# Kernel tuning notes

Hardware: AMD Instinct MI355X
Metric: run time of the kernel (lower is better)

The kernel has to match this reference:

```python
import jax, jax.numpy as jnp
import numpy as np

B, DEPTH, E, NH, HD = 32, 12, 768, 12, 64
IMG, PS, GRID = 224, 16, 14
N = GRID * GRID + 1  # 197 tokens incl. cls
EPS = 1e-5


def _rel_index(wh, ww):
    # BEiT relative position index, incl. cls-token rows/cols
    coords = np.stack(np.meshgrid(np.arange(wh), np.arange(ww), indexing='ij'))
    cf = coords.reshape(2, -1)
    rc = (cf[:, :, None] - cf[:, None, :]).transpose(1, 2, 0).astype(np.int64)
    rc[:, :, 0] += wh - 1
    rc[:, :, 1] += ww - 1
    rc[:, :, 0] *= 2 * ww - 1
    nrd = (2 * wh - 1) * (2 * ww - 1) + 3
    idx = np.zeros((wh * ww + 1, wh * ww + 1), dtype=np.int32)
    idx[1:, 1:] = rc.sum(-1)
    idx[0, :] = nrd - 3
    idx[:, 0] = nrd - 2
    idx[0, 0] = nrd - 1
    return jnp.asarray(idx)

REL_IDX = _rel_index(GRID, GRID)  # [197,197] int32 constant


def _ln(x, w, b):
    m = x.mean(-1, keepdims=True)
    v = ((x - m) ** 2).mean(-1, keepdims=True)
    return (x - m) * jax.lax.rsqrt(v + EPS) * w + b


def setup_inputs() -> dict:
    key = jax.random.key(0)
    ks = jax.random.split(key, 8)
    s = 0.02
    rn = lambda k, shape: jax.random.normal(k, shape, jnp.float32) * s
    D = DEPTH
    return {
        'x': jax.random.normal(ks[0], (B, 3, IMG, IMG), jnp.float32),
        'patch_w': rn(ks[1], (E, 3 * PS * PS)),
        'patch_b': jnp.zeros((E,), jnp.float32),
        'cls_token': jnp.zeros((1, 1, E), jnp.float32),
        'ln1_w': jnp.ones((D, E), jnp.float32),
        'ln1_b': jnp.zeros((D, E), jnp.float32),
        'qkv_w': rn(ks[2], (D, 3 * E, E)),
        'q_bias': jnp.zeros((D, E), jnp.float32),
        'v_bias': jnp.zeros((D, E), jnp.float32),
        'rel_table': rn(ks[3], (D, (2 * GRID - 1) ** 2 + 3, NH)),
        'proj_w': rn(ks[4], (D, E, E)),
        'proj_b': jnp.zeros((D, E), jnp.float32),
        'ln2_w': jnp.ones((D, E), jnp.float32),
        'ln2_b': jnp.zeros((D, E), jnp.float32),
        'fc1_w': rn(ks[5], (D, 4 * E, E)),
        'fc1_b': jnp.zeros((D, 4 * E), jnp.float32),
        'fc2_w': rn(ks[6], (D, E, 4 * E)),
        'fc2_b': jnp.zeros((D, E), jnp.float32),
        'fcn_w': jnp.ones((E,), jnp.float32),
        'fcn_b': jnp.zeros((E,), jnp.float32),
        'head_w': rn(ks[7], (1000, E)),
        'head_b': jnp.zeros((1000,), jnp.float32),
    }


def reference(x, patch_w, patch_b, cls_token, ln1_w, ln1_b, qkv_w, q_bias,
              v_bias, rel_table, proj_w, proj_b, ln2_w, ln2_b, fc1_w, fc1_b,
              fc2_w, fc2_b, fcn_w, fcn_b, head_w, head_b):
    b = x.shape[0]
    scale = HD ** -0.5
    # patch embed: stride-16 conv == patchify + matmul (weight flattened as [E, C*kh*kw])
    patches = x.reshape(b, 3, GRID, PS, GRID, PS).transpose(0, 2, 4, 1, 3, 5)
    patches = patches.reshape(b, GRID * GRID, 3 * PS * PS)
    tok = patches @ patch_w.T + patch_b
    tok = jnp.concatenate([jnp.broadcast_to(cls_token, (b, 1, E)), tok], axis=1)  # [B,197,E]

    params = dict(ln1_w=ln1_w, ln1_b=ln1_b, qkv_w=qkv_w, q_bias=q_bias,
                  v_bias=v_bias, rel_table=rel_table, proj_w=proj_w,
                  proj_b=proj_b, ln2_w=ln2_w, ln2_b=ln2_b, fc1_w=fc1_w,
                  fc1_b=fc1_b, fc2_w=fc2_w, fc2_b=fc2_b)

    def block(h, p):
        y = _ln(h, p['ln1_w'], p['ln1_b'])
        qkvb = jnp.concatenate([p['q_bias'], jnp.zeros_like(p['q_bias']), p['v_bias']])
        qkv = (y @ p['qkv_w'].T + qkvb).reshape(b, N, 3, NH, HD).transpose(2, 0, 3, 1, 4)
        q, k, v = qkv[0] * scale, qkv[1], qkv[2]  # [B,H,N,hd]
        bias = p['rel_table'][REL_IDX].transpose(2, 0, 1)  # [H,N,N]
        att = jax.nn.softmax(jnp.einsum('bhnd,bhmd->bhnm', q, k) + bias[None], axis=-1)
        o = jnp.einsum('bhnm,bhmd->bhnd', att, v).transpose(0, 2, 1, 3).reshape(b, N, E)
        h = h + o @ p['proj_w'].T + p['proj_b']
        y = _ln(h, p['ln2_w'], p['ln2_b'])
        y = jax.nn.gelu(y @ p['fc1_w'].T + p['fc1_b'], approximate=False)
        return h + y @ p['fc2_w'].T + p['fc2_b'], None

    tok, _ = jax.lax.scan(block, tok, params)
    feat = _ln(tok[:, 1:].mean(axis=1), fcn_w, fcn_b)  # mean pooling over patch tokens
    return feat @ head_w.T + head_b  # [B, 1000]
```

## Files before the change

kernel.cpp:

```cpp
#include <hip/hip_runtime.h>
#include <hip/hip_bf16.h>
#include <math.h>


typedef __hip_bfloat16 bf16;
using short8 = __attribute__((ext_vector_type(8))) short;
using f32x4  = __attribute__((ext_vector_type(4))) float;

#define NTOK 197
#define NHEAD 12
#define NPAD 224

#define S_QKV  1769472
#define S_PROJ 589824
#define S_FC   2359296
#define O_PROJ 1769472
#define O_FC1  2359296
#define O_FC2  4718592
#define W_TOT  7077888

#define GLD(gp, lp) __builtin_amdgcn_global_load_lds( \
    (const unsigned int __attribute__((address_space(1)))*)(gp), \
    (unsigned int __attribute__((address_space(3)))*)(lp), 16, 0, 0)

__global__ __launch_bounds__(256) void cvt_k(const float* __restrict__ src,
                                             bf16* __restrict__ dst, int n8) {
  int t = blockIdx.x * 256 + threadIdx.x;
  if (t >= n8) return;
  size_t i = (size_t)t * 8;
  float4 a = *(const float4*)(src + i);
  float4 b = *(const float4*)(src + i + 4);
  union { short8 v; bf16 e[8]; } u;
  u.e[0] = __float2bfloat16(a.x); u.e[1] = __float2bfloat16(a.y);
  u.e[2] = __float2bfloat16(a.z); u.e[3] = __float2bfloat16(a.w);
  u.e[4] = __float2bfloat16(b.x); u.e[5] = __float2bfloat16(b.y);
  u.e[6] = __float2bfloat16(b.z); u.e[7] = __float2bfloat16(b.w);
  *(short8*)(dst + i) = u.v;
}

__global__ __launch_bounds__(256) void cvt_layer_k(
    const float* __restrict__ qkvw, const float* __restrict__ projw,
    const float* __restrict__ fc1w, const float* __restrict__ fc2w,
    bf16* __restrict__ wl, int d) {
  size_t i = ((size_t)blockIdx.x * 256 + threadIdx.x) * 8;
  if (i >= W_TOT) return;
  const float* src;
  if (i < O_PROJ)      src = qkvw + (size_t)d * S_QKV + i;
  else if (i < O_FC1)  src = projw + (size_t)d * S_PROJ + (i - O_PROJ);
  else if (i < O_FC2)  src = fc1w + (size_t)d * S_FC + (i - O_FC1);
  else                 src = fc2w + (size_t)d * S_FC + (i - O_FC2);
  float4 a = *(const float4*)src;
  float4 b = *(const float4*)(src + 4);
  union { short8 v; bf16 e[8]; } u;
  u.e[0] = __float2bfloat16(a.x); u.e[1] = __float2bfloat16(a.y);
  u.e[2] = __float2bfloat16(a.z); u.e[3] = __float2bfloat16(a.w);
  u.e[4] = __float2bfloat16(b.x); u.e[5] = __float2bfloat16(b.y);
  u.e[6] = __float2bfloat16(b.z); u.e[7] = __float2bfloat16(b.w);
  *(short8*)(wl + i) = u.v;
}

__global__ __launch_bounds__(256) void patchify_k(const float* __restrict__ x,
                                                  bf16* __restrict__ patches) {
  int o = blockIdx.x * 256 + threadIdx.x;
  if (o >= 6272 * 768) return;
  int row = o / 768, col = o % 768;
  int b = row / 196, g = row % 196;
  int gh = g / 14, gw = g % 14;
  int c = col / 256, r = col % 256;
  int ph = r / 16, pw = r % 16;
  patches[o] = __float2bfloat16(
      x[(((size_t)b * 3 + c) * 224 + gh * 16 + ph) * 224 + gw * 16 + pw]);
}

__global__ __launch_bounds__(256) void clsfill_k(const float* __restrict__ cls,
                                                 float* __restrict__ h) {
  int i = blockIdx.x * 256 + threadIdx.x;
  if (i >= 32 * 768) return;
  int b = i / 768, e = i % 768;
  h[((size_t)b * 197) * 768 + e] = cls[e];
}

__global__ __launch_bounds__(256) void vtz_k(bf16* __restrict__ vt) {
  int i = blockIdx.x * 256 + threadIdx.x;
  if (i >= 32 * 12 * 64 * NPAD / 8) return;
  *(short8*)(vt + (size_t)i * 8) = (short8){0,0,0,0,0,0,0,0};
}

__device__ __forceinline__ int ridx(int n, int m) {
  if (n == 0) return (m == 0) ? 731 : 729;
  if (m == 0) return 730;
  int nh = (n - 1) / 14, nw = (n - 1) % 14;
  int mh = (m - 1) / 14, mw = (m - 1) % 14;
  return (nh - mh + 13) * 27 + (nw - mw + 13);
}

__global__ __launch_bounds__(256) void bias_k(const float* __restrict__ rel,
                                              float* __restrict__ biasT,
                                              int layer) {
  int idx = blockIdx.x * 256 + threadIdx.x;
  if (idx >= 12 * NPAD * 256) return;
  int h = idx / (NPAD * 256);
  int rem = idx % (NPAD * 256);
  int m = rem / 256, n = rem % 256;
  float v;
  if (m >= NTOK) {
    v = -1e30f;
  } else {
    int nn = min(n, NTOK - 1);
    v = rel[((size_t)layer * 732 + ridx(nn, m)) * 12 + h];
  }
  biasT[idx] = v;
}

template <int BIASMODE, bool DOGELU, bool DORES, bool REMAP, bool OUTBF16>
__global__ __launch_bounds__(256) void mm_k(
    const bf16* __restrict__ A, const bf16* __restrict__ W,
    const float* __restrict__ bias, const float* __restrict__ bias2,
    const float* __restrict__ Res, void* __restrict__ Cout,
    bf16* __restrict__ vtg, int M, int Nn, int K) {
  __shared__ bf16 As[4096];
  __shared__ bf16 Bs[4096];
  const int tid = threadIdx.x;
  const int lane = tid & 63;
  const int wave = tid >> 6;
  const int wr = wave >> 1, wc = wave & 1;
  const int row0 = blockIdx.x * 128, n0 = blockIdx.y * 128;
  const int srow = tid >> 2;
  const int scol = (tid & 3) * 8;
  const bf16* Ap = A + (size_t)(row0 + srow) * K + scol;
  const bf16* Wp = W + (size_t)(n0 + srow) * K + scol;
  const size_t gstep = (size_t)64 * K;
  const int r16 = lane & 15;
  const int kg = (lane >> 4) * 8;

  f32x4 acc[4][4];
#pragma unroll
  for (int m = 0; m < 4; m++)
#pragma unroll
    for (int n = 0; n < 4; n++) acc[m][n] = (f32x4){0.f, 0.f, 0.f, 0.f};

  for (int k0 = 0; k0 < K; k0 += 32) {
    __syncthreads();
    GLD(Ap, As + tid * 8);
    GLD(Ap + gstep, As + 2048 + tid * 8);
    GLD(Wp, Bs + tid * 8);
    GLD(Wp + gstep, Bs + 2048 + tid * 8);
    Ap += 32; Wp += 32;
    __syncthreads();

    short8 a[4], b[4];
#pragma unroll
    for (int m = 0; m < 4; m++)
      a[m] = *(const short8*)&As[(wr * 64 + m * 16 + r16) * 32 + kg];
#pragma unroll
    for (int n = 0; n < 4; n++)
      b[n] = *(const short8*)&Bs[(wc * 64 + n * 16 + r16) * 32 + kg];
#pragma unroll
    for (int m = 0; m < 4; m++)
#pragma unroll
      for (int n = 0; n < 4; n++)
        acc[m][n] = __builtin_amdgcn_mfma_f32_16x16x32_bf16(a[m], b[n], acc[m][n], 0, 0, 0);
  }

#pragma unroll
  for (int m = 0; m < 4; m++) {
    const int rbase = row0 + wr * 64 + m * 16 + (lane >> 4) * 4;
#pragma unroll
    for (int n = 0; n < 4; n++) {
      const int gc = n0 + wc * 64 + n * 16 + r16;
      f32x4 v = acc[m][n];
#pragma unroll
      for (int j = 0; j < 4; j++) {
        int gr = rbase + j;
        if (gr >= M) continue;
        float val = v[j];
        if (BIASMODE == 0) {
          val += bias[gc];
        } else {
          if (gc < 768) val += bias[gc];
          else if (gc >= 1536) val += bias2[gc - 1536];
        }
        if (DOGELU) val = 0.5f * val * (1.f + erff(val * 0.70710678118654752f));
        if (DORES) val += Res[(size_t)gr * Nn + gc];
        if (BIASMODE == 1 && gc >= 1536) {
          int ob = gr / 197;
          int nn = gr - ob * 197;
          int hd = gc - 1536;
          vtg[(((size_t)ob * 12 + (hd >> 6)) * 64 + (hd & 63)) * NPAD + nn] =
              __float2bfloat16(val);
        } else {
          int orow = REMAP ? (gr + gr / 196 + 1) : gr;
          if (OUTBF16)
            ((bf16*)Cout)[(size_t)orow * Nn + gc] = __float2bfloat16(val);
          else
            ((float*)Cout)[(size_t)orow * Nn + gc] = val;
        }
      }
    }
  }
}

__global__ __launch_bounds__(256) void ln_k(const float* __restrict__ in,
                                            bf16* __restrict__ outp,
                                            const float* __restrict__ w,
                                            const float* __restrict__ b,
                                            int rows) {
  int row = blockIdx.x * 4 + threadIdx.y;
  if (row >= rows) return;
  int lane = threadIdx.x;
  const float* xr = in + (size_t)row * 768;
  float v[12];
  float s = 0.f;
#pragma unroll
  for (int i = 0; i < 12; i++) { v[i] = xr[lane + i * 64]; s += v[i]; }
#pragma unroll
  for (int o = 32; o; o >>= 1) s += __shfl_xor(s, o);
  float mean = s * (1.f / 768.f);
  float var = 0.f;
#pragma unroll
  for (int i = 0; i < 12; i++) { float d = v[i] - mean; var += d * d; }
#pragma unroll
  for (int o = 32; o; o >>= 1) var += __shfl_xor(var, o);
  float rs = rsqrtf(var * (1.f / 768.f) + 1e-5f);
  bf16* orow = outp + (size_t)row * 768;
#pragma unroll
  for (int i = 0; i < 12; i++) {
    int e = lane + i * 64;
    orow[e] = __float2bfloat16((v[i] - mean) * rs * w[e] + b[e]);
  }
}

__device__ __forceinline__ unsigned pkbf(float a, float b) {
  union { bf16 h; unsigned short u; } ua, ub;
  ua.h = __float2bfloat16(a); ub.h = __float2bfloat16(b);
  return ((unsigned)ub.u << 16) | (unsigned)ua.u;
}

__global__ __launch_bounds__(256) void attn2_k(const bf16* __restrict__ qkvb,
                                               const bf16* __restrict__ vtg,
                                               const float* __restrict__ biasT,
                                               bf16* __restrict__ outp) {
  __shared__ bf16 Ks[NPAD * 64];
  __shared__ bf16 Vt[64 * NPAD];
  __shared__ bf16 Ps[4][64 * 32];
  __shared__ float denl[4][64];

  const int bh = blockIdx.x;
  const int b = bh / 12, h = bh % 12;
  const int tid = threadIdx.x;
  const int wave = tid >> 6, lane = tid & 63;
  const int l15 = lane & 15, lg = lane >> 4;
  const int qbase = wave * 64;

  const bf16* vsrc = vtg + (size_t)bh * 64 * NPAD;
#pragma unroll
  for (int i = 0; i < 7; i++) {
    int c = i * 256 + tid;
    GLD(vsrc + c * 8, Vt + c * 8);
  }
#pragma unroll
  for (int i = 0; i < 7; i++) {
    int slot = i * 256 + tid;
    int r = slot >> 3, c8 = (slot & 7) * 8;
    int rg = min(r, NTOK - 1);
    short8 kv = *(const short8*)(qkvb + (size_t)(b * NTOK + rg) * 2304 + 768 + h * 64 + c8);
    int byte = (r * 128 + c8 * 2) ^ ((r & 7) << 4);
    *(short8*)((char*)Ks + byte) = kv;
  }
  short8 qf[4][2];
#pragma unroll
  for (int nf = 0; nf < 4; nf++) {
    int n = qbase + nf * 16 + l15;
    const bf16* qp = qkvb + (size_t)(b * NTOK + min(n, NTOK - 1)) * 2304 + h * 64;
    qf[nf][0] = *(const short8*)(qp + lg * 8);
    qf[nf][1] = *(const short8*)(qp + 32 + lg * 8);
  }
  __syncthreads();

  f32x4 Oacc[4][4];
#pragma unroll
  for (int i = 0; i < 4; i++)
#pragma unroll
    for (int j = 0; j < 4; j++) Oacc[i][j] = (f32x4){0.f, 0.f, 0.f, 0.f};
  float den[4] = {0.f, 0.f, 0.f, 0.f};
  const float* bT = biasT + (size_t)h * NPAD * 256;
  char* pw = (char*)&Ps[wave][0];

  for (int c = 0; c < 7; c++) {
    const int m0 = c * 32;
    f32x4 st[2][4];
#pragma unroll
    for (int mf = 0; mf < 2; mf++)
#pragma unroll
      for (int nf = 0; nf < 4; nf++) st[mf][nf] = (f32x4){0.f, 0.f, 0.f, 0.f};
#pragma unroll
    for (int kk = 0; kk < 2; kk++) {
      short8 af[2];
#pragma unroll
      for (int mf = 0; mf < 2; mf++) {
        int m = m0 + mf * 16 + l15;
        int byte = (m * 128 + kk * 64 + lg * 16) ^ ((m & 7) << 4);
        af[mf] = *(const short8*)((const char*)Ks + byte);
      }
#pragma unroll
      for (int mf = 0; mf < 2; mf++)
#pragma unroll
        for (int nf = 0; nf < 4; nf++)
          st[mf][nf] = __builtin_amdgcn_mfma_f32_16x16x32_bf16(af[mf], qf[nf][kk], st[mf][nf], 0, 0, 0);
    }
#pragma unroll
    for (int mf = 0; mf < 2; mf++) {
      int mrow = m0 + mf * 16 + lg * 4;
#pragma unroll
      for (int nf = 0; nf < 4; nf++) {
        int n = qbase + nf * 16 + l15;
        float p0 = __expf(st[mf][nf][0] * 0.125f + bT[(mrow + 0) * 256 + n]);
        float p1 = __expf(st[mf][nf][1] * 0.125f + bT[(mrow + 1) * 256 + n]);
        float p2 = __expf(st[mf][nf][2] * 0.125f + bT[(mrow + 2) * 256 + n]);
        float p3 = __expf(st[mf][nf][3] * 0.125f + bT[(mrow + 3) * 256 + n]);
        den[nf] += (p0 + p1) + (p2 + p3);
        int nl = nf * 16 + l15;
        int byte = (nl * 64 + (mf * 16 + lg * 4) * 2) ^ ((nl & 7) << 4);
        *(unsigned*)(pw + byte) = pkbf(p0, p1);
        *(unsigned*)(pw + byte + 4) = pkbf(p2, p3);
      }
    }
    short8 pa[4], vb[4];
#pragma unroll
    for (int nf = 0; nf < 4; nf++) {
      int nl = nf * 16 + l15;
      int byte = (nl * 64 + lg * 16) ^ ((nl & 7) << 4);
      pa[nf] = *(const short8*)((const char*)pw + byte);
    }
#pragma unroll
    for (int df = 0; df < 4; df++) {
      int d = df * 16 + l15;
      vb[df] = *(const short8*)(Vt + d * NPAD + m0 + lg * 8);
    }
#pragma unroll
    for (int nf = 0; nf < 4; nf++)
#pragma unroll
      for (int df = 0; df < 4; df++)
        Oacc[nf][df] = __builtin_amdgcn_mfma_f32_16x16x32_bf16(pa[nf], vb[df], Oacc[nf][df], 0, 0, 0);
  }

#pragma unroll
  for (int nf = 0; nf < 4; nf++) {
    den[nf] += __shfl_xor(den[nf], 16);
    den[nf] += __shfl_xor(den[nf], 32);
    denl[wave][nf * 16 + l15] = den[nf];
  }
  float inv[4][4];
#pragma unroll
  for (int nf = 0; nf < 4; nf++)
#pragma unroll
    for (int j = 0; j < 4; j++)
      inv[nf][j] = 1.f / denl[wave][nf * 16 + lg * 4 + j];
#pragma unroll
  for (int nf = 0; nf < 4; nf++) {
#pragma unroll
    for (int df = 0; df < 4; df++) {
#pragma unroll
      for (int j = 0; j < 4; j++) {
        int n = qbase + nf * 16 + lg * 4 + j;
        if (n < NTOK)
          outp[(size_t)(b * NTOK + n) * 768 + h * 64 + df * 16 + l15] =
              __float2bfloat16(Oacc[nf][df][j] * inv[nf][j]);
      }
    }
  }
}

__device__ __forceinline__ float block_sum(float v, float* sm4) {
#pragma unroll
  for (int o = 32; o; o >>= 1) v += __shfl_down(v, o);
  __syncthreads();
  if ((threadIdx.x & 63) == 0) sm4[threadIdx.x >> 6] = v;
  __syncthreads();
  return sm4[0] + sm4[1] + sm4[2] + sm4[3];
}

__global__ __launch_bounds__(256) void pool_ln_k(const float* __restrict__ h,
                                                 const float* __restrict__ w,
                                                 const float* __restrict__ bi,
                                                 float* __restrict__ feat) {
  __shared__ float sm4[4];
  int b = blockIdx.x, tid = threadIdx.x;
  float vals[3];
  float local = 0.f;
#pragma unroll
  for (int j = 0; j < 3; j++) {
    int e = tid + j * 256;
    float s = 0.f;
    for (int nn = 1; nn < 197; nn++) s += h[((size_t)(b * 197 + nn)) * 768 + e];
    s *= (1.f / 196.f);
    vals[j] = s;
    local += s;
  }
  float tot = block_sum(local, sm4);
  float mean = tot * (1.f / 768.f);
  float lv = 0.f;
#pragma unroll
  for (int j = 0; j < 3; j++) { float d = vals[j] - mean; lv += d * d; }
  float vtot = block_sum(lv, sm4);
  float rs = rsqrtf(vtot * (1.f / 768.f) + 1e-5f);
#pragma unroll
  for (int j = 0; j < 3; j++) {
    int e = tid + j * 256;
    feat[(size_t)b * 768 + e] = (vals[j] - mean) * rs * w[e] + bi[e];
  }
}

__global__ __launch_bounds__(256) void head_k(const float* __restrict__ A,
                                              const float* __restrict__ W,
                                              const float* __restrict__ bias,
                                              float* __restrict__ C,
                                              int M, int Nn, int K) {
  __shared__ float As[16][64 + 4];
  __shared__ float Bs[16][64 + 4];
  int tid = threadIdx.x;
  int tx = tid & 15, ty = tid >> 4;
  int row0 = blockIdx.x * 64, n0 = blockIdx.y * 64;
  int lrow = tid >> 2;
  int kq = (tid & 3) * 4;
  float acc[4][4];
#pragma unroll
  for (int i = 0; i < 4; i++)
#pragma unroll
    for (int j = 0; j < 4; j++) acc[i][j] = 0.f;
  for (int k0 = 0; k0 < K; k0 += 16) {
    float4 av = make_float4(0.f, 0.f, 0.f, 0.f);
    if (row0 + lrow < M) av = *(const float4*)&A[(size_t)(row0 + lrow) * K + k0 + kq];
    As[kq + 0][lrow] = av.x; As[kq + 1][lrow] = av.y;
    As[kq + 2][lrow] = av.z; As[kq + 3][lrow] = av.w;
    float4 bv = make_float4(0.f, 0.f, 0.f, 0.f);
    if (n0 + lrow < Nn) bv = *(const float4*)&W[(size_t)(n0 + lrow) * K + k0 + kq];
    Bs[kq + 0][lrow] = bv.x; Bs[kq + 1][lrow] = bv.y;
    Bs[kq + 2][lrow] = bv.z; Bs[kq + 3][lrow] = bv.w;
    __syncthreads();
#pragma unroll
    for (int kk = 0; kk < 16; kk++) {
      float4 a = *(const float4*)&As[kk][ty * 4];
      float4 b = *(const float4*)&Bs[kk][tx * 4];
      float aa[4] = {a.x, a.y, a.z, a.w};
      float bb[4] = {b.x, b.y, b.z, b.w};
#pragma unroll
      for (int i = 0; i < 4; i++)
#pragma unroll
        for (int j = 0; j < 4; j++) acc[i][j] = fmaf(aa[i], bb[j], acc[i][j]);
    }
    __syncthreads();
  }
#pragma unroll
  for (int i = 0; i < 4; i++) {
    int gr = row0 + ty * 4 + i;
    if (gr >= M) continue;
#pragma unroll
    for (int j = 0; j < 4; j++) {
      int gc = n0 + tx * 4 + j;
      if (gc >= Nn) continue;
      C[(size_t)gr * Nn + gc] = acc[i][j] + bias[gc];
    }
  }
}

extern "C" void kernel_launch(void* const* d_in, const int* in_sizes, int n_in,
                              void* d_out, int out_size, void* d_ws, size_t ws_size,
                              hipStream_t stream) {
  const float* x       = (const float*)d_in[0];
  const float* patch_w = (const float*)d_in[1];
  const float* patch_b = (const float*)d_in[2];
  const float* cls_tok = (const float*)d_in[3];
  const float* ln1_w   = (const float*)d_in[4];
  const float* ln1_b   = (const float*)d_in[5];
  const float* qkv_w   = (const float*)d_in[6];
  const float* q_bias  = (const float*)d_in[7];
  const float* v_bias  = (const float*)d_in[8];
  const float* rel_tab = (const float*)d_in[9];
  const float* proj_w  = (const float*)d_in[10];
  const float* proj_b  = (const float*)d_in[11];
  const float* ln2_w   = (const float*)d_in[12];
  const float* ln2_b   = (const float*)d_in[13];
  const float* fc1_w   = (const float*)d_in[14];
  const float* fc1_b   = (const float*)d_in[15];
  const float* fc2_w   = (const float*)d_in[16];
  const float* fc2_b   = (const float*)d_in[17];
  const float* fcn_w   = (const float*)d_in[18];
  const float* fcn_b   = (const float*)d_in[19];
  const float* head_w  = (const float*)d_in[20];
  const float* head_b  = (const float*)d_in[21];
  float* outp = (float*)d_out;

  char* wsb = (char*)d_ws;
  float* h    = (float*)wsb;  wsb += 19365888;
  bf16* bigb  = (bf16*)wsb;   wsb += 29048832;
  bf16* yb    = (bf16*)wsb;   wsb += 9830400;
  bf16* hid   = (bf16*)wsb;   wsb += 39321600;
  bf16* wl    = (bf16*)wsb;   wsb += 14155776;
  bf16* vt_g  = (bf16*)wsb;   wsb += 11010048;
  float* biasT = (float*)wsb; wsb += 2752512;
  float* feat = (float*)wsb;

  const int M = 6304;

  vtz_k<<<2688, 256, 0, stream>>>(vt_g);
  patchify_k<<<(6272 * 768 + 255) / 256, 256, 0, stream>>>(x, hid);
  cvt_k<<<(589824 / 8 + 255) / 256, 256, 0, stream>>>(patch_w, wl, 589824 / 8);
  {
    dim3 g(49, 6);
    mm_k<0, false, false, true, false><<<g, 256, 0, stream>>>(
        hid, wl, patch_b, nullptr, nullptr, h, nullptr, 6272, 768, 768);
  }
  clsfill_k<<<(32 * 768 + 255) / 256, 256, 0, stream>>>(cls_tok, h);

  for (int d = 0; d < 12; d++) {
    cvt_layer_k<<<W_TOT / 8 / 256, 256, 0, stream>>>(qkv_w, proj_w, fc1_w, fc2_w, wl, d);
    bias_k<<<(12 * NPAD * 256) / 256, 256, 0, stream>>>(rel_tab, biasT, d);
    ln_k<<<dim3((M + 3) / 4), dim3(64, 4), 0, stream>>>(h, yb, ln1_w + d * 768, ln1_b + d * 768, M);
    {
      dim3 g(50, 18);
      mm_k<1, false, false, false, true><<<g, 256, 0, stream>>>(
          yb, wl, q_bias + d * 768, v_bias + d * 768, nullptr, bigb, vt_g, M, 2304, 768);
    }
    attn2_k<<<32 * NHEAD, 256, 0, stream>>>(bigb, vt_g, biasT, yb);
    {
      dim3 g(50, 6);
      mm_k<0, false, true, false, false><<<g, 256, 0, stream>>>(
          yb, wl + O_PROJ, proj_b + d * 768, nullptr, h, h, nullptr, M, 768, 768);
    }
    ln_k<<<dim3((M + 3) / 4), dim3(64, 4), 0, stream>>>(h, yb, ln2_w + d * 768, ln2_b + d * 768, M);
    {
      dim3 g(50, 24);
      mm_k<0, true, false, false, true><<<g, 256, 0, stream>>>(
          yb, wl + O_FC1, fc1_b + d * 3072, nullptr, nullptr, hid, nullptr, M, 3072, 768);
    }
    {
      dim3 g(50, 6);
      mm_k<0, false, true, false, false><<<g, 256, 0, stream>>>(
          hid, wl + O_FC2, fc2_b + d * 768, nullptr, h, h, nullptr, M, 768, 3072);
    }
  }

  pool_ln_k<<<32, 256, 0, stream>>>(h, fcn_w, fcn_b, feat);
  {
    dim3 g(1, (1000 + 63) / 64);
    head_k<<<g, 256, 0, stream>>>(feat, head_w, head_b, outp, 32, 1000, 768);
  }
}
```

Before: 4.069 ms.

## Double-buffer LDS tiles in GEMM kernel to overlap loads with MFMA

Replaces the single shared-memory A/B tile with two buffers and prefetches the next K-slice via global_load_lds while the current slice is consumed by MFMAs. This cuts the per-iteration barriers from two to one and aims to hide global memory latency. It doubles LDS usage per block, which may reduce occupancy.

New measurement: 3.650 ms. -10.3%, faster.

```diff
diff --git a/kernel.cpp b/kernel.cpp
--- a/kernel.cpp
+++ b/kernel.cpp
@@ -118,8 +118,7 @@
     const float* __restrict__ bias, const float* __restrict__ bias2,
     const float* __restrict__ Res, void* __restrict__ Cout,
     bf16* __restrict__ vtg, int M, int Nn, int K) {
-  __shared__ bf16 As[4096];
-  __shared__ bf16 Bs[4096];
+  __shared__ bf16 lds[2][8192];
   const int tid = threadIdx.x;
   const int lane = tid & 63;
   const int wave = tid >> 6;
@@ -139,15 +138,29 @@
 #pragma unroll
     for (int n = 0; n < 4; n++) acc[m][n] = (f32x4){0.f, 0.f, 0.f, 0.f};
 
-  for (int k0 = 0; k0 < K; k0 += 32) {
-    __syncthreads();
-    GLD(Ap, As + tid * 8);
-    GLD(Ap + gstep, As + 2048 + tid * 8);
-    GLD(Wp, Bs + tid * 8);
-    GLD(Wp + gstep, Bs + 2048 + tid * 8);
-    Ap += 32; Wp += 32;
-    __syncthreads();
-
+  const int nt = K >> 5;
+  {
+    bf16* dst = lds[0];
+    GLD(Ap, dst + tid * 8);
+    GLD(Ap + gstep, dst + 2048 + tid * 8);
+    GLD(Wp, dst + 4096 + tid * 8);
+    GLD(Wp + 4096  - 4096 + gstep, dst + 6144 + tid * 8);
+  }
+  __syncthreads();
+
+  for (int t = 0; t < nt; ++t) {
+    const int cur = t & 1;
+    if (t + 1 < nt) {
+      bf16* dst = lds[cur ^ 1];
+      const bf16* a = Ap + (t + 1) * 32;
+      const bf16* w = Wp + (t + 1) * 32;
+      GLD(a, dst + tid * 8);
+      GLD(a + gstep, dst + 2048 + tid * 8);
+      GLD(w, dst + 4096 + tid * 8);
+      GLD(w + gstep, dst + 6144 + tid * 8);
+    }
+    const bf16* As = lds[cur];
+    const bf16* Bs = lds[cur] + 4096;
     short8 a[4], b[4];
 #pragma unroll
     for (int m = 0; m < 4; m++)
@@ -160,6 +173,7 @@
 #pragma unroll
       for (int n = 0; n < 4; n++)
         acc[m][n] = __builtin_amdgcn_mfma_f32_16x16x32_bf16(a[m], b[n], acc[m][n], 0, 0, 0);
+    __syncthreads();
   }
 
 #pragma unroll
```

## Replace GEMM with 256-row, 8-wave, 4-stage pipelined swizzled-LDS kernel

Applied to the files above, without the earlier changes.

Replaces the 128x128 single-buffered bf16 MFMA GEMM with a 512-thread kernel using 256-row tiles and 128- or 256-wide column tiles. Tiles stream through a 4-deep LDS ring via direct global-to-LDS loads with explicit vmcnt waits, and an XOR swizzle avoids LDS bank conflicts. MFMA blocks are wrapped in s_setprio. The goal is to hide global-load latency and raise data reuse per tile. In exchange, LDS use per block is large and wide tiles give fewer blocks (225–300) than the GPU has CUs, which risks underutilisation on some GEMMs.

After: 4.020 ms. No clear change (-1.2%).

```diff
diff --git a/kernel.cpp b/kernel.cpp
--- a/kernel.cpp
+++ b/kernel.cpp
@@ -112,88 +112,142 @@
   biasT[idx] = v;
 }
 
-template <int BIASMODE, bool DOGELU, bool DORES, bool REMAP, bool OUTBF16>
-__global__ __launch_bounds__(256) void mm_k(
+template <int EPI, int BN>
+__global__ __launch_bounds__(512, 2) void mm8_k(
     const bf16* __restrict__ A, const bf16* __restrict__ W,
     const float* __restrict__ bias, const float* __restrict__ bias2,
     const float* __restrict__ Res, void* __restrict__ Cout,
     bf16* __restrict__ vtg, int M, int Nn, int K) {
-  __shared__ bf16 As[4096];
-  __shared__ bf16 Bs[4096];
+  constexpr int BNW = BN / 4;
+  constexpr int NFR = BN / 64;
+  constexpr int ATILE = 16384;
+  constexpr int BTILE = BN * 64;
+  constexpr int BUFB = ATILE + BTILE;
+  constexpr int LDB = BTILE / 8192;
+  __shared__ __attribute__((aligned(16))) char lds[4 * BUFB];
+
   const int tid = threadIdx.x;
   const int lane = tid & 63;
   const int wave = tid >> 6;
-  const int wr = wave >> 1, wc = wave & 1;
-  const int row0 = blockIdx.x * 128, n0 = blockIdx.y * 128;
-  const int srow = tid >> 2;
-  const int scol = (tid & 3) * 8;
-  const bf16* Ap = A + (size_t)(row0 + srow) * K + scol;
-  const bf16* Wp = W + (size_t)(n0 + srow) * K + scol;
-  const size_t gstep = (size_t)64 * K;
-  const int r16 = lane & 15;
-  const int kg = (lane >> 4) * 8;
-
-  f32x4 acc[4][4];
-#pragma unroll
-  for (int m = 0; m < 4; m++)
-#pragma unroll
-    for (int n = 0; n < 4; n++) acc[m][n] = (f32x4){0.f, 0.f, 0.f, 0.f};
-
-  for (int k0 = 0; k0 < K; k0 += 32) {
-    __syncthreads();
-    GLD(Ap, As + tid * 8);
-    GLD(Ap + gstep, As + 2048 + tid * 8);
-    GLD(Wp, Bs + tid * 8);
-    GLD(Wp + gstep, Bs + 2048 + tid * 8);
-    Ap += 32; Wp += 32;
-    __syncthreads();
-
-    short8 a[4], b[4];
-#pragma unroll
-    for (int m = 0; m < 4; m++)
-      a[m] = *(const short8*)&As[(wr * 64 + m * 16 + r16) * 32 + kg];
-#pragma unroll
-    for (int n = 0; n < 4; n++)
-      b[n] = *(const short8*)&Bs[(wc * 64 + n * 16 + r16) * 32 + kg];
-#pragma unroll
-    for (int m = 0; m < 4; m++)
-#pragma unroll
-      for (int n = 0; n < 4; n++)
+  const int wr = wave >> 2;
+  const int wc = wave & 3;
+  const int row0 = blockIdx.x * 256, n0 = blockIdx.y * BN;
+  const int l15 = lane & 15, lg = lane >> 4;
+  const int nt = K >> 5;
+
+  const bf16* gA[2]; int dstA[2];
+  const bf16* gB[LDB]; int dstB[LDB];
+#pragma unroll
+  for (int i = 0; i < 2; i++) {
+    int s = i * 8192 + tid * 16;
+    int L = s >> 7; int u = s ^ ((L & 7) << 4);
+    int r = 2 * L + ((u >> 6) & 1); int c = (u & 63) >> 1;
+    gA[i] = A + (size_t)(row0 + r) * K + c;
+    dstA[i] = s;
+  }
+#pragma unroll
+  for (int i = 0; i < LDB; i++) {
+    int s = i * 8192 + tid * 16;
+    int L = s >> 7; int u = s ^ ((L & 7) << 4);
+    int r = 2 * L + ((u >> 6) & 1); int c = (u & 63) >> 1;
+    gB[i] = W + (size_t)(n0 + r) * K + c;
+    dstB[i] = ATILE + s;
+  }
+
+  int offA[8], offB[NFR];
+#pragma unroll
+  for (int m = 0; m < 8; m++) {
+    int r = wr * 128 + m * 16 + l15;
+    int L = r >> 1;
+    offA[m] = ((L << 7) | ((r & 1) << 6) | (lg * 16)) ^ ((L & 7) << 4);
+  }
+#pragma unroll
+  for (int n = 0; n < NFR; n++) {
+    int r = wc * BNW + n * 16 + l15;
+    int L = r >> 1;
+    offB[n] = ATILE + (((L << 7) | ((r & 1) << 6) | (lg * 16)) ^ ((L & 7) << 4));
+  }
+
+  f32x4 acc[8][NFR];
+#pragma unroll
+  for (int m = 0; m < 8; m++)
+#pragma unroll
+    for (int n = 0; n < NFR; n++) acc[m][n] = (f32x4){0.f, 0.f, 0.f, 0.f};
+
+#define STAGE(tt, bb)                                              \
+  {                                                                \
+    _Pragma("unroll")                                              \
+    for (int i = 0; i < 2; i++)                                    \
+      GLD(gA[i] + (tt) * 32, lds + (bb) * BUFB + dstA[i]);         \
+    _Pragma("unroll")                                              \
+    for (int i = 0; i < LDB; i++)                                  \
+      GLD(gB[i] + (tt) * 32, lds + (bb) * BUFB + dstB[i]);         \
+  }
+
+  STAGE(0, 0); STAGE(1, 1); STAGE(2, 2);
+  if constexpr (LDB == 2) asm volatile("s_waitcnt vmcnt(8)" ::: "memory");
+  else                    asm volatile("s_waitcnt vmcnt(6)" ::: "memory");
+  __builtin_amdgcn_s_barrier();
+  __builtin_amdgcn_sched_barrier(0);
+
+  for (int t = 0; t < nt; ++t) {
+    const int tc = (t + 3 < nt) ? (t + 3) : (nt - 1);
+    STAGE(tc, (t + 3) & 3);
+    const char* base = lds + (t & 3) * BUFB;
+    short8 b[NFR], a[8];
+#pragma unroll
+    for (int n = 0; n < NFR; n++) b[n] = *(const short8*)(base + offB[n]);
+#pragma unroll
+    for (int m = 0; m < 8; m++) a[m] = *(const short8*)(base + offA[m]);
+    __builtin_amdgcn_s_setprio(1);
+#pragma unroll
+    for (int m = 0; m < 8; m++)
+#pragma unroll
+      for (int n = 0; n < NFR; n++)
         acc[m][n] = __builtin_amdgcn_mfma_f32_16x16x32_bf16(a[m], b[n], acc[m][n], 0, 0, 0);
-  }
-
-#pragma unroll
-  for (int m = 0; m < 4; m++) {
-    const int rbase = row0 + wr * 64 + m * 16 + (lane >> 4) * 4;
-#pragma unroll
-    for (int n = 0; n < 4; n++) {
-      const int gc = n0 + wc * 64 + n * 16 + r16;
+    __builtin_amdgcn_s_setprio(0);
+    if constexpr (LDB == 2) asm volatile("s_waitcnt vmcnt(8)" ::: "memory");
+    else                    asm volatile("s_waitcnt vmcnt(6)" ::: "memory");
+    __builtin_amdgcn_s_barrier();
+    __builtin_amdgcn_sched_barrier(0);
+  }
+#undef STAGE
+
+#pragma unroll
+  for (int m = 0; m < 8; m++) {
+    const int rbase = row0 + wr * 128 + m * 16 + lg * 4;
+#pragma unroll
+    for (int n = 0; n < NFR; n++) {
+      const int gc = n0 + wc * BNW + n * 16 + l15;
       f32x4 v = acc[m][n];
 #pragma unroll
       for (int j = 0; j < 4; j++) {
         int gr = rbase + j;
         if (gr >= M) continue;
         float val = v[j];
-        if (BIASMODE == 0) {
-          val += bias[gc];
-        } else {
+        if (EPI == 1) {
           if (gc < 768) val += bias[gc];
           else if (gc >= 1536) val += bias2[gc - 1536];
+        } else {
+          val += bias[gc];
         }
-        if (DOGELU) val = 0.5f * val * (1.f + erff(val * 0.70710678118654752f));
-        if (DORES) val += Res[(size_t)gr * Nn + gc];
-        if (BIASMODE == 1 && gc >= 1536) {
-          int ob = gr / 197;
-          int nn = gr - ob * 197;
-          int hd = gc - 1536;
-          vtg[(((size_t)ob * 12 + (hd >> 6)) * 64 + (hd & 63)) * NPAD + nn] =
-              __float2bfloat16(val);
+        if (EPI == 3) val = 0.5f * val * (1.f + erff(val * 0.70710678118654752f));
+        if (EPI == 2) val += Res[(size_t)gr * Nn + gc];
+        if (EPI == 1) {
+          if (gc >= 1536) {
+            int ob = gr / 197, nn = gr - ob * 197, hd = gc - 1536;
+            vtg[(((size_t)ob * 12 + (hd >> 6)) * 64 + (hd & 63)) * NPAD + nn] =
+                __float2bfloat16(val);
+          } else {
+            ((bf16*)Cout)[(size_t)gr * Nn + gc] = __float2bfloat16(val);
+          }
+        } else if (EPI == 0) {
+          int orow = gr + gr / 196 + 1;
+          ((float*)Cout)[(size_t)orow * Nn + gc] = val;
+        } else if (EPI == 2) {
+          ((float*)Cout)[(size_t)gr * Nn + gc] = val;
         } else {
-          int orow = REMAP ? (gr + gr / 196 + 1) : gr;
-          if (OUTBF16)
-            ((bf16*)Cout)[(size_t)orow * Nn + gc] = __float2bfloat16(val);
-          else
-            ((float*)Cout)[(size_t)orow * Nn + gc] = val;
+          ((bf16*)Cout)[(size_t)gr * Nn + gc] = __float2bfloat16(val);
         }
       }
     }
@@ -506,39 +560,24 @@
   vtz_k<<<2688, 256, 0, stream>>>(vt_g);
   patchify_k<<<(6272 * 768 + 255) / 256, 256, 0, stream>>>(x, hid);
   cvt_k<<<(589824 / 8 + 255) / 256, 256, 0, stream>>>(patch_w, wl, 589824 / 8);
-  {
-    dim3 g(49, 6);
-    mm_k<0, false, false, true, false><<<g, 256, 0, stream>>>(
-        hid, wl, patch_b, nullptr, nullptr, h, nullptr, 6272, 768, 768);
-  }
+  mm8_k<0, 128><<<dim3(25, 6), 512, 0, stream>>>(
+      hid, wl, patch_b, nullptr, nullptr, h, nullptr, 6272, 768, 768);
   clsfill_k<<<(32 * 768 + 255) / 256, 256, 0, stream>>>(cls_tok, h);
 
   for (int d = 0; d < 12; d++) {
     cvt_layer_k<<<W_TOT / 8 / 256, 256, 0, stream>>>(qkv_w, proj_w, fc1_w, fc2_w, wl, d);
     bias_k<<<(12 * NPAD * 256) / 256, 256, 0, stream>>>(rel_tab, biasT, d);
     ln_k<<<dim3((M + 3) / 4), dim3(64, 4), 0, stream>>>(h, yb, ln1_w + d * 768, ln1_b + d * 768, M);
-    {
-      dim3 g(50, 18);
-      mm_k<1, false, false, false, true><<<g, 256, 0, stream>>>(
-          yb, wl, q_bias + d * 768, v_bias + d * 768, nullptr, bigb, vt_g, M, 2304, 768);
-    }
+    mm8_k<1, 256><<<dim3(25, 9), 512, 0, stream>>>(
+        yb, wl, q_bias + d * 768, v_bias + d * 768, nullptr, bigb, vt_g, M, 2304, 768);
     attn2_k<<<32 * NHEAD, 256, 0, stream>>>(bigb, vt_g, biasT, yb);
-    {
-      dim3 g(50, 6);
-      mm_k<0, false, true, false, false><<<g, 256, 0, stream>>>(
-          yb, wl + O_PROJ, proj_b + d * 768, nullptr, h, h, nullptr, M, 768, 768);
-    }
+    mm8_k<2, 128><<<dim3(25, 6), 512, 0, stream>>>(
+        yb, wl + O_PROJ, proj_b + d * 768, nullptr, h, h, nullptr, M, 768, 768);
     ln_k<<<dim3((M + 3) / 4), dim3(64, 4), 0, stream>>>(h, yb, ln2_w + d * 768, ln2_b + d * 768, M);
-    {
-      dim3 g(50, 24);
-      mm_k<0, true, false, false, true><<<g, 256, 0, stream>>>(
-          yb, wl + O_FC1, fc1_b + d * 3072, nullptr, nullptr, hid, nullptr, M, 3072, 768);
-    }
-    {
-      dim3 g(50, 6);
-      mm_k<0, false, true, false, false><<<g, 256, 0, stream>>>(
-          hid, wl + O_FC2, fc2_b + d * 768, nullptr, h, h, nullptr, M, 768, 3072);
-    }
+    mm8_k<3, 256><<<dim3(25, 12), 512, 0, stream>>>(
+        yb, wl + O_FC1, fc1_b + d * 3072, nullptr, nullptr, hid, nullptr, M, 3072, 768);
+    mm8_k<2, 128><<<dim3(25, 6), 512, 0, stream>>>(
+        hid, wl + O_FC2, fc2_b + d * 768, nullptr, h, h, nullptr, M, 768, 3072);
   }
 
   pool_ln_k<<<32, 256, 0, stream>>>(h, fcn_w, fcn_b, feat);
```

## Replace GEMM kernel with triple-buffered swizzled pipelines and split-K fc2

Applied to the files above, without the earlier changes.

The single synchronous GEMM kernel is replaced by two software-pipelined variants. Both use three LDS buffers with async global-to-LDS prefetch two k-steps ahead, an XOR-swizzled LDS layout, and raised MFMA priority. QKV and fc1 move to 256x128 tiles with 512 threads; fc2 becomes a two-way split-K writing fp32 partials, followed by a separate reduction kernel that adds bias and residual. The goal is to hide global-load latency and cut LDS bank conflicts. In exchange it adds an extra reduction pass over partials and places those partials in a reused scratch buffer that spills past its nominal size into the adjacent yb buffer.

Result: faster. 3.435 ms (-15.6%).

```diff
diff --git a/kernel.cpp b/kernel.cpp
--- a/kernel.cpp
+++ b/kernel.cpp
@@ -112,26 +112,46 @@
   biasT[idx] = v;
 }
 
-template <int BIASMODE, bool DOGELU, bool DORES, bool REMAP, bool OUTBF16>
-__global__ __launch_bounds__(256) void mm_k(
+template <int EPI>
+__global__ __launch_bounds__(512, 4) void mm256_k(
     const bf16* __restrict__ A, const bf16* __restrict__ W,
     const float* __restrict__ bias, const float* __restrict__ bias2,
-    const float* __restrict__ Res, void* __restrict__ Cout,
-    bf16* __restrict__ vtg, int M, int Nn, int K) {
-  __shared__ bf16 As[4096];
-  __shared__ bf16 Bs[4096];
+    void* __restrict__ Cout, bf16* __restrict__ vtg, float* __restrict__ part,
+    int M, int Nn, int K, int lda) {
+  constexpr int BUFSZ = 24576;
+  __shared__ __attribute__((aligned(16))) char lds[3 * BUFSZ];
   const int tid = threadIdx.x;
-  const int lane = tid & 63;
-  const int wave = tid >> 6;
+  const int lane = tid & 63, wave = tid >> 6;
   const int wr = wave >> 1, wc = wave & 1;
-  const int row0 = blockIdx.x * 128, n0 = blockIdx.y * 128;
-  const int srow = tid >> 2;
-  const int scol = (tid & 3) * 8;
-  const bf16* Ap = A + (size_t)(row0 + srow) * K + scol;
-  const bf16* Wp = W + (size_t)(n0 + srow) * K + scol;
-  const size_t gstep = (size_t)64 * K;
-  const int r16 = lane & 15;
-  const int kg = (lane >> 4) * 8;
+  const int l15 = lane & 15, lg = lane >> 4;
+  const int row0 = blockIdx.x * 256, n0 = blockIdx.y * 128;
+  const int kofs = blockIdx.z * K;
+  const int nt = K >> 5, ntm1 = nt - 1;
+
+  const bf16 *gA0, *gA1, *gB0;
+  int dA0, dA1, dB0;
+  {
+    int s = tid * 16;
+    int r = s >> 6, cl = ((s >> 4) & 3) ^ ((r >> 1) & 3);
+    gA0 = A + (size_t)(row0 + r) * lda + kofs + cl * 8;  dA0 = s;
+    s = 8192 + tid * 16;
+    r = s >> 6; cl = ((s >> 4) & 3) ^ ((r >> 1) & 3);
+    gA1 = A + (size_t)(row0 + r) * lda + kofs + cl * 8;  dA1 = s;
+    s = tid * 16;
+    r = s >> 6; cl = ((s >> 4) & 3) ^ ((r >> 1) & 3);
+    gB0 = W + (size_t)(n0 + r) * lda + kofs + cl * 8;    dB0 = 16384 + s;
+  }
+  int oA[4], oB[4];
+#pragma unroll
+  for (int m = 0; m < 4; m++) {
+    int r = wr * 64 + m * 16 + l15;
+    oA[m] = (r << 6) | ((lg ^ ((r >> 1) & 3)) << 4);
+  }
+#pragma unroll
+  for (int n = 0; n < 4; n++) {
+    int r = wc * 64 + n * 16 + l15;
+    oB[n] = 16384 + ((r << 6) | ((lg ^ ((r >> 1) & 3)) << 4));
+  }
 
   f32x4 acc[4][4];
 #pragma unroll
@@ -139,65 +159,197 @@
 #pragma unroll
     for (int n = 0; n < 4; n++) acc[m][n] = (f32x4){0.f, 0.f, 0.f, 0.f};
 
-  for (int k0 = 0; k0 < K; k0 += 32) {
-    __syncthreads();
-    GLD(Ap, As + tid * 8);
-    GLD(Ap + gstep, As + 2048 + tid * 8);
-    GLD(Wp, Bs + tid * 8);
-    GLD(Wp + gstep, Bs + 2048 + tid * 8);
-    Ap += 32; Wp += 32;
-    __syncthreads();
-
-    short8 a[4], b[4];
-#pragma unroll
-    for (int m = 0; m < 4; m++)
-      a[m] = *(const short8*)&As[(wr * 64 + m * 16 + r16) * 32 + kg];
-#pragma unroll
-    for (int n = 0; n < 4; n++)
-      b[n] = *(const short8*)&Bs[(wc * 64 + n * 16 + r16) * 32 + kg];
-#pragma unroll
-    for (int m = 0; m < 4; m++)
-#pragma unroll
-      for (int n = 0; n < 4; n++)
-        acc[m][n] = __builtin_amdgcn_mfma_f32_16x16x32_bf16(a[m], b[n], acc[m][n], 0, 0, 0);
-  }
+  GLD(gA0, lds + dA0); GLD(gA1, lds + dA1); GLD(gB0, lds + dB0);
+  GLD(gA0 + 32, lds + BUFSZ + dA0); GLD(gA1 + 32, lds + BUFSZ + dA1);
+  GLD(gB0 + 32, lds + BUFSZ + dB0);
+  asm volatile("s_waitcnt vmcnt(3)" ::: "memory");
+  __builtin_amdgcn_s_barrier();
+  __builtin_amdgcn_sched_barrier(0);
+
+#define MB(RB, WB, tt)                                                        \
+  {                                                                           \
+    int ks = (tt) + 2; if (ks > ntm1) ks = ntm1; ks <<= 5;                    \
+    char* wb = lds + (WB) * BUFSZ;                                            \
+    GLD(gA0 + ks, wb + dA0); GLD(gA1 + ks, wb + dA1);                         \
+    GLD(gB0 + ks, wb + dB0);                                                  \
+    const char* rb = lds + (RB) * BUFSZ;                                      \
+    short8 a[4], b[4];                                                        \
+    _Pragma("unroll") for (int m = 0; m < 4; m++)                             \
+      a[m] = *(const short8*)(rb + oA[m]);                                    \
+    _Pragma("unroll") for (int n = 0; n < 4; n++)                             \
+      b[n] = *(const short8*)(rb + oB[n]);                                    \
+    __builtin_amdgcn_s_setprio(1);                                            \
+    _Pragma("unroll") for (int m = 0; m < 4; m++)                             \
+      _Pragma("unroll") for (int n = 0; n < 4; n++)                           \
+        acc[m][n] = __builtin_amdgcn_mfma_f32_16x16x32_bf16(a[m], b[n], acc[m][n], 0, 0, 0); \
+    __builtin_amdgcn_s_setprio(0);                                            \
+    __builtin_amdgcn_sched_barrier(0);                                        \
+    asm volatile("s_waitcnt vmcnt(2)" ::: "memory");                          \
+    __builtin_amdgcn_s_barrier();                                             \
+    __builtin_amdgcn_sched_barrier(0);                                        \
+  }
+
+  for (int t = 0; t < nt; t += 3) {
+    MB(0, 2, t); MB(1, 0, t + 1); MB(2, 1, t + 2);
+  }
+#undef MB
+  asm volatile("s_waitcnt vmcnt(0)" ::: "memory");
 
 #pragma unroll
   for (int m = 0; m < 4; m++) {
-    const int rbase = row0 + wr * 64 + m * 16 + (lane >> 4) * 4;
+    const int rbase = row0 + wr * 64 + m * 16 + lg * 4;
 #pragma unroll
     for (int n = 0; n < 4; n++) {
-      const int gc = n0 + wc * 64 + n * 16 + r16;
+      const int gc = n0 + wc * 64 + n * 16 + l15;
       f32x4 v = acc[m][n];
 #pragma unroll
       for (int j = 0; j < 4; j++) {
         int gr = rbase + j;
         if (gr >= M) continue;
         float val = v[j];
-        if (BIASMODE == 0) {
-          val += bias[gc];
-        } else {
+        if (EPI == 1) {
           if (gc < 768) val += bias[gc];
           else if (gc >= 1536) val += bias2[gc - 1536];
-        }
-        if (DOGELU) val = 0.5f * val * (1.f + erff(val * 0.70710678118654752f));
-        if (DORES) val += Res[(size_t)gr * Nn + gc];
-        if (BIASMODE == 1 && gc >= 1536) {
-          int ob = gr / 197;
-          int nn = gr - ob * 197;
-          int hd = gc - 1536;
-          vtg[(((size_t)ob * 12 + (hd >> 6)) * 64 + (hd & 63)) * NPAD + nn] =
-              __float2bfloat16(val);
+          if (gc >= 1536) {
+            int ob = gr / 197, nn = gr - ob * 197, hd = gc - 1536;
+            vtg[(((size_t)ob * 12 + (hd >> 6)) * 64 + (hd & 63)) * NPAD + nn] =
+                __float2bfloat16(val);
+          } else {
+            ((bf16*)Cout)[(size_t)gr * Nn + gc] = __float2bfloat16(val);
+          }
+        } else if (EPI == 3) {
+          val += bias[gc];
+          val = 0.5f * val * (1.f + erff(val * 0.70710678118654752f));
+          ((bf16*)Cout)[(size_t)gr * Nn + gc] = __float2bfloat16(val);
         } else {
-          int orow = REMAP ? (gr + gr / 196 + 1) : gr;
-          if (OUTBF16)
-            ((bf16*)Cout)[(size_t)orow * Nn + gc] = __float2bfloat16(val);
-          else
-            ((float*)Cout)[(size_t)orow * Nn + gc] = val;
+          part[(size_t)blockIdx.z * M * Nn + (size_t)gr * Nn + gc] = val;
         }
       }
     }
   }
+}
+
+template <int EPI>
+__global__ __launch_bounds__(256, 3) void mm128_k(
+    const bf16* __restrict__ A, const bf16* __restrict__ W,
+    const float* __restrict__ bias, const float* __restrict__ Res,
+    void* __restrict__ Cout, int M, int Nn, int K) {
+  constexpr int BUFSZ = 16384;
+  __shared__ __attribute__((aligned(16))) char lds[3 * BUFSZ];
+  const int tid = threadIdx.x;
+  const int lane = tid & 63, wave = tid >> 6;
+  const int wr = wave >> 1, wc = wave & 1;
+  const int l15 = lane & 15, lg = lane >> 4;
+  const int row0 = blockIdx.x * 128, n0 = blockIdx.y * 128;
+  const int nt = K >> 5, ntm1 = nt - 1;
+
+  const bf16 *gA0, *gA1, *gB0, *gB1;
+  int dA0, dA1, dB0, dB1;
+  {
+    int s = tid * 16;
+    int r = s >> 6, cl = ((s >> 4) & 3) ^ ((r >> 1) & 3);
+    gA0 = A + (size_t)(row0 + r) * K + cl * 8;  dA0 = s;
+    s = 4096 + tid * 16;
+    r = s >> 6; cl = ((s >> 4) & 3) ^ ((r >> 1) & 3);
+    gA1 = A + (size_t)(row0 + r) * K + cl * 8;  dA1 = s;
+    s = tid * 16;
+    r = s >> 6; cl = ((s >> 4) & 3) ^ ((r >> 1) & 3);
+    gB0 = W + (size_t)(n0 + r) * K + cl * 8;    dB0 = 8192 + s;
+    s = 4096 + tid * 16;
+    r = s >> 6; cl = ((s >> 4) & 3) ^ ((r >> 1) & 3);
+    gB1 = W + (size_t)(n0 + r) * K + cl * 8;    dB1 = 8192 + s;
+  }
+  int oA[4], oB[4];
+#pragma unroll
+  for (int m = 0; m < 4; m++) {
+    int r = wr * 64 + m * 16 + l15;
+    oA[m] = (r << 6) | ((lg ^ ((r >> 1) & 3)) << 4);
+  }
+#pragma unroll
+  for (int n = 0; n < 4; n++) {
+    int r = wc * 64 + n * 16 + l15;
+    oB[n] = 8192 + ((r << 6) | ((lg ^ ((r >> 1) & 3)) << 4));
+  }
+
+  f32x4 acc[4][4];
+#pragma unroll
+  for (int m = 0; m < 4; m++)
+#pragma unroll
+    for (int n = 0; n < 4; n++) acc[m][n] = (f32x4){0.f, 0.f, 0.f, 0.f};
+
+  GLD(gA0, lds + dA0); GLD(gA1, lds + dA1);
+  GLD(gB0, lds + dB0); GLD(gB1, lds + dB1);
+  GLD(gA0 + 32, lds + BUFSZ + dA0); GLD(gA1 + 32, lds + BUFSZ + dA1);
+  GLD(gB0 + 32, lds + BUFSZ + dB0); GLD(gB1 + 32, lds + BUFSZ + dB1);
+  asm volatile("s_waitcnt vmcnt(4)" ::: "memory");
+  __builtin_amdgcn_s_barrier();
+  __builtin_amdgcn_sched_barrier(0);
+
+#define MB(RB, WB, tt)                                                        \
+  {                                                                           \
+    int ks = (tt) + 2; if (ks > ntm1) ks = ntm1; ks <<= 5;                    \
+    char* wb = lds + (WB) * BUFSZ;                                            \
+    GLD(gA0 + ks, wb + dA0); GLD(gA1 + ks, wb + dA1);                         \
+    GLD(gB0 + ks, wb + dB0); GLD(gB1 + ks, wb + dB1);                         \
+    const char* rb = lds + (RB) * BUFSZ;                                      \
+    short8 a[4], b[4];                                                        \
+    _Pragma("unroll") for (int m = 0; m < 4; m++)                             \
+      a[m] = *(const short8*)(rb + oA[m]);                                    \
+    _Pragma("unroll") for (int n = 0; n < 4; n++)                             \
+      b[n] = *(const short8*)(rb + oB[n]);                                    \
+    __builtin_amdgcn_s_setprio(1);                                            \
+    _Pragma("unroll") for (int m = 0; m < 4; m++)                             \
+      _Pragma("unroll") for (int n = 0; n < 4; n++)                           \
+        acc[m][n] = __builtin_amdgcn_mfma_f32_16x16x32_bf16(a[m], b[n], acc[m][n], 0, 0, 0); \
+    __builtin_amdgcn_s_setprio(0);                                            \
+    __builtin_amdgcn_sched_barrier(0);                                        \
+    asm volatile("s_waitcnt vmcnt(3)" ::: "memory");                          \
+    __builtin_amdgcn_s_barrier();                                             \
+    __builtin_amdgcn_sched_barrier(0);                                        \
+  }
+
+  for (int t = 0; t < nt; t += 3) {
+    MB(0, 2, t); MB(1, 0, t + 1); MB(2, 1, t + 2);
+  }
+#undef MB
+  asm volatile("s_waitcnt vmcnt(0)" ::: "memory");
+
+#pragma unroll
+  for (int m = 0; m < 4; m++) {
+    const int rbase = row0 + wr * 64 + m * 16 + lg * 4;
+#pragma unroll
+    for (int n = 0; n < 4; n++) {
+      const int gc = n0 + wc * 64 + n * 16 + l15;
+      f32x4 v = acc[m][n];
+#pragma unroll
+      for (int j = 0; j < 4; j++) {
+        int gr = rbase + j;
+        if (gr >= M) continue;
+        float val = v[j] + bias[gc];
+        if (EPI == 2) val += Res[(size_t)gr * Nn + gc];
+        int orow = (EPI == 0) ? (gr + gr / 196 + 1) : gr;
+        ((float*)Cout)[(size_t)orow * Nn + gc] = val;
+      }
+    }
+  }
+}
+
+__global__ __launch_bounds__(256) void fc2red_k(const float* __restrict__ part,
+                                                const float* __restrict__ bias,
+                                                float* __restrict__ h) {
+  int i = blockIdx.x * 256 + threadIdx.x;
+  if (i >= 6304 * 768 / 4) return;
+  size_t o = (size_t)i * 4;
+  float4 p0 = *(const float4*)(part + o);
+  float4 p1 = *(const float4*)(part + (size_t)6304 * 768 + o);
+  float4 hv = *(const float4*)(h + o);
+  const float4 bv = *(const float4*)(bias + (int)(o % 768));
+  float4 r;
+  r.x = p0.x + p1.x + hv.x + bv.x;
+  r.y = p0.y + p1.y + hv.y + bv.y;
+  r.z = p0.z + p1.z + hv.z + bv.z;
+  r.w = p0.w + p1.w + hv.w + bv.w;
+  *(float4*)(h + o) = r;
 }
 
 __global__ __launch_bounds__(256) void ln_k(const float* __restrict__ in,
@@ -500,45 +652,35 @@
   bf16* vt_g  = (bf16*)wsb;   wsb += 11010048;
   float* biasT = (float*)wsb; wsb += 2752512;
   float* feat = (float*)wsb;
+  float* part = (float*)bigb;
 
   const int M = 6304;
 
   vtz_k<<<2688, 256, 0, stream>>>(vt_g);
   patchify_k<<<(6272 * 768 + 255) / 256, 256, 0, stream>>>(x, hid);
   cvt_k<<<(589824 / 8 + 255) / 256, 256, 0, stream>>>(patch_w, wl, 589824 / 8);
-  {
-    dim3 g(49, 6);
-    mm_k<0, false, false, true, false><<<g, 256, 0, stream>>>(
-        hid, wl, patch_b, nullptr, nullptr, h, nullptr, 6272, 768, 768);
-  }
+  mm128_k<0><<<dim3(49, 6), 256, 0, stream>>>(
+      hid, wl, patch_b, nullptr, h, 6272, 768, 768);
   clsfill_k<<<(32 * 768 + 255) / 256, 256, 0, stream>>>(cls_tok, h);
 
   for (int d = 0; d < 12; d++) {
     cvt_layer_k<<<W_TOT / 8 / 256, 256, 0, stream>>>(qkv_w, proj_w, fc1_w, fc2_w, wl, d);
     bias_k<<<(12 * NPAD * 256) / 256, 256, 0, stream>>>(rel_tab, biasT, d);
     ln_k<<<dim3((M + 3) / 4), dim3(64, 4), 0, stream>>>(h, yb, ln1_w + d * 768, ln1_b + d * 768, M);
-    {
-      dim3 g(50, 18);
-      mm_k<1, false, false, false, true><<<g, 256, 0, stream>>>(
-          yb, wl, q_bias + d * 768, v_bias + d * 768, nullptr, bigb, vt_g, M, 2304, 768);
-    }
+    mm256_k<1><<<dim3(25, 18), 512, 0, stream>>>(
+        yb, wl, q_bias + d * 768, v_bias + d * 768, bigb, vt_g, nullptr,
+        M, 2304, 768, 768);
     attn2_k<<<32 * NHEAD, 256, 0, stream>>>(bigb, vt_g, biasT, yb);
-    {
-      dim3 g(50, 6);
-      mm_k<0, false, true, false, false><<<g, 256, 0, stream>>>(
-          yb, wl + O_PROJ, proj_b + d * 768, nullptr, h, h, nullptr, M, 768, 768);
-    }
+    mm128_k<2><<<dim3(50, 6), 256, 0, stream>>>(
+        yb, wl + O_PROJ, proj_b + d * 768, h, h, M, 768, 768);
     ln_k<<<dim3((M + 3) / 4), dim3(64, 4), 0, stream>>>(h, yb, ln2_w + d * 768, ln2_b + d * 768, M);
-    {
-      dim3 g(50, 24);
-      mm_k<0, true, false, false, true><<<g, 256, 0, stream>>>(
-          yb, wl + O_FC1, fc1_b + d * 3072, nullptr, nullptr, hid, nullptr, M, 3072, 768);
-    }
-    {
-      dim3 g(50, 6);
-      mm_k<0, false, true, false, false><<<g, 256, 0, stream>>>(
-          hid, wl + O_FC2, fc2_b + d * 768, nullptr, h, h, nullptr, M, 768, 3072);
-    }
+    mm256_k<3><<<dim3(25, 24), 512, 0, stream>>>(
+        yb, wl + O_FC1, fc1_b + d * 3072, nullptr, hid, nullptr, nullptr,
+        M, 3072, 768, 768);
+    mm256_k<4><<<dim3(25, 6, 2), 512, 0, stream>>>(
+        hid, wl + O_FC2, nullptr, nullptr, nullptr, nullptr, part,
+        M, 768, 1536, 3072);
+    fc2red_k<<<(6304 * 768 / 4 + 255) / 256, 256, 0, stream>>>(part, fc2_b + d * 768, h);
   }
 
   pool_ln_k<<<32, 256, 0, stream>>>(h, fcn_w, fcn_b, feat);
```
